# Performance work log

Hardware: AMD Instinct MI355X
Metric: run time of the kernel (lower is better)

Reference implementation:

```python
import jax, jax.numpy as jnp
import numpy as np

N, E, F_IN, H, C = 50000, 800000, 256, 64, 40
NEG_SLOPE = 0.2


def setup_inputs() -> dict:
    key = jax.random.key(0)
    ks = jax.random.split(key, 16)
    sc = lambda fan: 1.0 / np.sqrt(fan)
    return {
        "x": jax.random.normal(ks[0], (N, F_IN), dtype=jnp.float32),
        "edge_index": jax.random.randint(ks[1], (2, E), 0, N, dtype=jnp.int64),
        "W1l": jax.random.normal(ks[2], (F_IN, H), dtype=jnp.float32) * sc(F_IN),
        "b1l": jnp.zeros((H,), jnp.float32),
        "W1r": jax.random.normal(ks[3], (F_IN, H), dtype=jnp.float32) * sc(F_IN),
        "b1r": jnp.zeros((H,), jnp.float32),
        "att1": jax.random.normal(ks[4], (H,), dtype=jnp.float32) * sc(H),
        "bias1": jnp.zeros((H,), jnp.float32),
        "lin1_W": jax.random.normal(ks[5], (F_IN, H), dtype=jnp.float32) * sc(F_IN),
        "lin1_b": jnp.zeros((H,), jnp.float32),
        "W2l": jax.random.normal(ks[6], (H, C), dtype=jnp.float32) * sc(H),
        "b2l": jnp.zeros((C,), jnp.float32),
        "W2r": jax.random.normal(ks[7], (H, C), dtype=jnp.float32) * sc(H),
        "b2r": jnp.zeros((C,), jnp.float32),
        "att2": jax.random.normal(ks[8], (C,), dtype=jnp.float32) * sc(C),
        "bias2": jnp.zeros((C,), jnp.float32),
        "lin2_W": jax.random.normal(ks[9], (H, C), dtype=jnp.float32) * sc(H),
        "lin2_b": jnp.zeros((C,), jnp.float32),
    }


def gatv2_layer(x, src, dst, Wl, bl, Wr, br, att, bias, n):
    # PyG GATv2Conv, heads=1: xl = lin_l(x) (source), xr = lin_r(x) (target)
    xl = x @ Wl + bl                               # [n, out]
    xr = x @ Wr + br                               # [n, out]
    m = xl[src] + xr[dst]                          # [E, out] per-edge gather
    e = jax.nn.leaky_relu(m, NEG_SLOPE) @ att      # [E] attention logits
    # segment softmax over destination nodes (self-loops guarantee nonempty segments)
    emax = jax.ops.segment_max(e, dst, num_segments=n)
    ee = jnp.exp(e - emax[dst])
    denom = jax.ops.segment_sum(ee, dst, num_segments=n)
    alpha = ee / denom[dst]                        # [E]
    out = jax.ops.segment_sum(alpha[:, None] * xl[src], dst, num_segments=n)
    return out + bias


def reference(x, edge_index, W1l, b1l, W1r, b1r, att1, bias1, lin1_W, lin1_b,
              W2l, b2l, W2r, b2r, att2, bias2, lin2_W, lin2_b):
    n = x.shape[0]
    loops = jnp.arange(n, dtype=edge_index.dtype)
    src = jnp.concatenate([edge_index[0], loops])  # add_self_loops=True (PyG default)
    dst = jnp.concatenate([edge_index[1], loops])
    h = jax.nn.relu(gatv2_layer(x, src, dst, W1l, b1l, W1r, b1r, att1, bias1, n)
                    + x @ lin1_W + lin1_b)
    o = (gatv2_layer(h, src, dst, W2l, b2l, W2r, b2r, att2, bias2, n)
         + h @ lin2_W + lin2_b)
    return jax.nn.log_softmax(o, axis=1), edge_index
```

## Files before the change

kernel.cpp:

```cpp
#include <hip/hip_runtime.h>
#include <cmath>

#define NN 50000
#define NP 50048
#define NE 800000
#define CD 40
#define NEG_SLOPE 0.2f
#define NITEMS (NE + NN)
#define CHUNK 2048
#define NCH 416
#define NBKT 391
#define BCAP 3072
#define GB1 782
#define TB1 (3 * 64 * 256)
#define TB2 (3 * 64 * 64)
#define WPB 240

typedef __attribute__((ext_vector_type(8))) short s16x8;
typedef __attribute__((ext_vector_type(4))) float f32x4;
typedef __attribute__((ext_vector_type(2))) float f32x2;

__device__ __forceinline__ f32x2 pk_fma(f32x2 a, f32x2 b, f32x2 c) {
#if __has_builtin(__builtin_elementwise_fma)
  return __builtin_elementwise_fma(a, b, c);
#else
  f32x2 r; r[0] = fmaf(a[0], b[0], c[0]); r[1] = fmaf(a[1], b[1], c[1]); return r;
#endif
}
__device__ __forceinline__ f32x2 pk_max(f32x2 a, f32x2 b) {
#if __has_builtin(__builtin_elementwise_max)
  return __builtin_elementwise_max(a, b);
#else
  f32x2 r; r[0] = fmaxf(a[0], b[0]); r[1] = fmaxf(a[1], b[1]); return r;
#endif
}

__device__ __forceinline__ short f2bf(float x) {
  unsigned u = __builtin_bit_cast(unsigned, x);
  u += 0x7fffu + ((u >> 16) & 1u);
  return (short)(u >> 16);
}
__device__ __forceinline__ unsigned pack2(float lo, float hi) {
  return (unsigned)(unsigned short)f2bf(lo) | ((unsigned)(unsigned short)f2bf(hi) << 16);
}
__device__ __forceinline__ float bf2f_lo(unsigned v) {
  return __builtin_bit_cast(float, v << 16);
}
__device__ __forceinline__ float bf2f_hi(unsigned v) {
  return __builtin_bit_cast(float, v & 0xffff0000u);
}
__device__ __forceinline__ void unp8(uint4 v, f32x2* f) {
  f[0] = (f32x2){bf2f_lo(v.x), bf2f_hi(v.x)};
  f[1] = (f32x2){bf2f_lo(v.y), bf2f_hi(v.y)};
  f[2] = (f32x2){bf2f_lo(v.z), bf2f_hi(v.z)};
  f[3] = (f32x2){bf2f_lo(v.w), bf2f_hi(v.w)};
}
__device__ __forceinline__ uint4 zero4() {
  uint4 z; z.x = 0u; z.y = 0u; z.z = 0u; z.w = 0u; return z;
}

__global__ __launch_bounds__(256) void prep_bin(const float* __restrict__ W1l,
                                                const float* __restrict__ W1r,
                                                const float* __restrict__ L1,
                                                const float* __restrict__ W2l,
                                                const float* __restrict__ W2r,
                                                const float* __restrict__ L2,
                                                short* __restrict__ Wp1,
                                                short* __restrict__ Wp2,
                                                const int* __restrict__ ei,
                                                float* __restrict__ outE,
                                                int* __restrict__ gcur,
                                                unsigned* __restrict__ rec) {
  const int tid = threadIdx.x;
  if (blockIdx.x < WPB) {
    int e = blockIdx.x * 256 + tid;
    if (e < TB1) {
      int kb = e / 6144, r = e % 6144;
      int w = r / 2048, r2 = r % 2048;
      int t = r2 / 512, r3 = r2 % 512;
      int lane = r3 / 8, j = r3 % 8;
      int n = t * 16 + (lane & 15);
      int k = kb * 32 + (lane >> 4) * 8 + j;
      const float* W = (w == 0) ? W1l : (w == 1) ? W1r : L1;
      Wp1[e] = f2bf(W[k * 64 + n]);
    } else {
      e -= TB1;
      int kb = e / 6144, r = e % 6144;
      int w = r / 2048, r2 = r % 2048;
      int t = r2 / 512, r3 = r2 % 512;
      int lane = r3 / 8, j = r3 % 8;
      int n = t * 16 + (lane & 15);
      int k = kb * 32 + (lane >> 4) * 8 + j;
      const float* W = (w == 0) ? W2l : (w == 1) ? W2r : L2;
      Wp2[e] = (n < 40) ? f2bf(W[k * 40 + n]) : (short)0;
    }
    return;
  }
  __shared__ unsigned sorted[CHUNK];
  __shared__ int hist[512];
  __shared__ int bcur[512];
  __shared__ int gbase[512];
  const int base = (blockIdx.x - WPB) * CHUNK;
  for (int t = tid; t < 512; t += 256) { hist[t] = 0; bcur[t] = 0; gbase[t] = 0; }
  __syncthreads();
  unsigned key[CHUNK / 256];
#pragma unroll
  for (int u = 0; u < CHUNK / 256; ++u) {
    const int j = base + u * 256 + tid;
    unsigned k = 0xFFFFFFFFu;
    if (j < NITEMS) {
      int s, d;
      if (j < NE) {
        s = ei[j]; d = ei[NE + j];
        outE[j] = (float)s; outE[NE + j] = (float)d;
      } else {
        s = j - NE; d = s;
      }
      k = ((unsigned)d << 16) | (unsigned)s;
      atomicAdd(&hist[k >> 23], 1);
    }
    key[u] = k;
  }
  __syncthreads();
  if (tid < 64) {
    int carry = 0;
#pragma unroll
    for (int c = 0; c < 8; ++c) {
      int v = hist[c * 64 + tid];
      int inc = v;
#pragma unroll
      for (int off = 1; off < 64; off <<= 1) {
        int tt = __shfl_up(inc, off, 64);
        if (tid >= off) inc += tt;
      }
      hist[c * 64 + tid] = carry + inc - v;
      carry += __shfl(inc, 63, 64);
    }
  }
  __syncthreads();
#pragma unroll
  for (int u = 0; u < CHUNK / 256; ++u) {
    const unsigned k = key[u];
    if (k != 0xFFFFFFFFu) {
      const int b = k >> 23;
      sorted[hist[b] + atomicAdd(&bcur[b], 1)] = k;
    }
  }
  __syncthreads();
  for (int t = tid; t < NBKT; t += 256) {
    const int c = bcur[t];
    if (c > 0) gbase[t] = atomicAdd(&gcur[t], c);
  }
  __syncthreads();
  const int cnt = min(CHUNK, NITEMS - base);
  for (int i = tid; i < cnt; i += 256) {
    const unsigned k = sorted[i];
    const int b = k >> 23;
    const int p = gbase[b] + (i - hist[b]);
    if (p < BCAP) rec[(size_t)b * BCAP + p] = k;
  }
}

__device__ __forceinline__ void gemm1_body(int bid, const float* __restrict__ X,
                                           const short* __restrict__ Wp,
                                           const float* __restrict__ B0,
                                           const float* __restrict__ B1,
                                           const float* __restrict__ B2,
                                           unsigned short* __restrict__ Y0,
                                           unsigned short* __restrict__ Y1,
                                           unsigned short* __restrict__ Y2) {
  const int lane = threadIdx.x & 63;
  const int wave = threadIdx.x >> 6;
  const int r0 = bid * 64 + wave * 16;
  const int m = lane & 15;
  const int q = lane >> 4;
  f32x4 acc[3][4] = {};
  const float* a0 = X + (size_t)min(r0 + m, NN - 1) * 256 + q * 8;
  const short* bp = Wp + lane * 8;
  float4 v0 = *reinterpret_cast<const float4*>(a0);
  float4 v1 = *reinterpret_cast<const float4*>(a0 + 4);
#pragma unroll
  for (int kb = 0; kb < 8; ++kb) {
    s16x8 bf[12];
#pragma unroll
    for (int i = 0; i < 12; ++i)
      bf[i] = *reinterpret_cast<const s16x8*>(bp + (size_t)(kb * 12 + i) * 512);
    s16x8 af;
    af[0] = f2bf(v0.x); af[1] = f2bf(v0.y); af[2] = f2bf(v0.z); af[3] = f2bf(v0.w);
    af[4] = f2bf(v1.x); af[5] = f2bf(v1.y); af[6] = f2bf(v1.z); af[7] = f2bf(v1.w);
    if (kb < 7) {
      v0 = *reinterpret_cast<const float4*>(a0 + (kb + 1) * 32);
      v1 = *reinterpret_cast<const float4*>(a0 + (kb + 1) * 32 + 4);
    }
#pragma unroll
    for (int i = 0; i < 12; ++i)
      acc[i >> 2][i & 3] = __builtin_amdgcn_mfma_f32_16x16x32_bf16(
          af, bf[i], acc[i >> 2][i & 3], 0, 0, 0);
  }
#pragma unroll
  for (int w = 0; w < 3; ++w) {
    const float* B = (w == 0) ? B0 : (w == 1) ? B1 : B2;
    unsigned short* Y = (w == 0) ? Y0 : (w == 1) ? Y1 : Y2;
#pragma unroll
    for (int t = 0; t < 4; ++t) {
      const int c = t * 16 + m;
      const float bv = B[c];
#pragma unroll
      for (int rg = 0; rg < 4; ++rg) {
        const int row = r0 + q * 4 + rg;
        if (row < NN)
          Y[(size_t)row * 64 + c] = (unsigned short)f2bf(acc[w][t][rg] + bv);
      }
    }
  }
}

__global__ __launch_bounds__(256, 3) void build_gemm1(
    const float* __restrict__ X, const short* __restrict__ Wp1,
    const float* __restrict__ B0, const float* __restrict__ B1,
    const float* __restrict__ B2, unsigned short* __restrict__ Y0,
    unsigned short* __restrict__ Y1, unsigned short* __restrict__ Y2,
    const int* __restrict__ gcur, const unsigned* __restrict__ rec,
    int* __restrict__ offsets, unsigned short* __restrict__ csr16) {
  if (blockIdx.x < GB1) {
    gemm1_body(blockIdx.x, X, Wp1, B0, B1, B2, Y0, Y1, Y2);
    return;
  }
  const int b = blockIdx.x - GB1;
  const int tid = threadIdx.x;
  __shared__ unsigned recs[BCAP];
  __shared__ int red[256];
  __shared__ int cnt[128];
  __shared__ int sc[128];
  __shared__ int cur[128];
  int acc = 0;
  for (int t = tid; t < NBKT; t += 256)
    if (t < b) acc += gcur[t];
  red[tid] = acc;
  __syncthreads();
#pragma unroll
  for (int off = 128; off >= 1; off >>= 1) {
    if (tid < off) red[tid] += red[tid + off];
    __syncthreads();
  }
  const int base = red[0];
  const int Tb = min(gcur[b], BCAP);
  if (tid < 128) cnt[tid] = 0;
  __syncthreads();
  for (int i = tid; i < Tb; i += 256) {
    const unsigned k = rec[(size_t)b * BCAP + i];
    recs[i] = k;
    atomicAdd(&cnt[(k >> 16) & 127], 1);
  }
  __syncthreads();
  if (tid < 128) sc[tid] = cnt[tid];
  __syncthreads();
#pragma unroll
  for (int off = 1; off < 128; off <<= 1) {
    int v = (tid < 128 && tid >= off) ? sc[tid - off] : 0;
    __syncthreads();
    if (tid < 128) sc[tid] += v;
    __syncthreads();
  }
  if (tid < 128) {
    const int n = b * 128 + tid;
    if (n < NN) offsets[n + 1] = base + sc[tid];
    cur[tid] = sc[tid] - cnt[tid];
  }
  if (b == 0 && tid == 0) {
    offsets[0] = 0;
#pragma unroll
    for (int i = 0; i < 8; ++i) csr16[NITEMS + i] = 0;
  }
  __syncthreads();
  for (int i = tid; i < Tb; i += 256) {
    const unsigned k = recs[i];
    const int p = atomicAdd(&cur[(k >> 16) & 127], 1);
    csr16[base + p] = (unsigned short)(k & 0xFFFFu);
  }
}

__global__ __launch_bounds__(256, 2) void gemm2(const short* __restrict__ Xb,
                                                const short* __restrict__ Wp,
                                                const float* __restrict__ B0,
                                                const float* __restrict__ B1,
                                                const float* __restrict__ B2,
                                                unsigned short* __restrict__ Y0,
                                                unsigned short* __restrict__ Y1,
                                                unsigned short* __restrict__ Y2) {
  const int lane = threadIdx.x & 63;
  const int wave = threadIdx.x >> 6;
  const int r0 = blockIdx.x * 64 + wave * 16;
  const int m = lane & 15;
  const int q = lane >> 4;
  f32x4 acc[3][3] = {};
  const short* a0 = Xb + (size_t)(r0 + m) * 64 + q * 8;
  const short* bp = Wp + lane * 8;
#pragma unroll
  for (int kb = 0; kb < 2; ++kb) {
    s16x8 bf[9];
#pragma unroll
    for (int w = 0; w < 3; ++w)
#pragma unroll
      for (int t = 0; t < 3; ++t)
        bf[w * 3 + t] =
            *reinterpret_cast<const s16x8*>(bp + (size_t)(kb * 12 + w * 4 + t) * 512);
    const s16x8 af = *reinterpret_cast<const s16x8*>(a0 + kb * 32);
#pragma unroll
    for (int w = 0; w < 3; ++w)
#pragma unroll
      for (int t = 0; t < 3; ++t)
        acc[w][t] = __builtin_amdgcn_mfma_f32_16x16x32_bf16(af, bf[w * 3 + t],
                                                            acc[w][t], 0, 0, 0);
  }
#pragma unroll
  for (int w = 0; w < 3; ++w) {
    const float* B = (w == 0) ? B0 : (w == 1) ? B1 : B2;
    unsigned short* Y = (w == 0) ? Y0 : (w == 1) ? Y1 : Y2;
#pragma unroll
    for (int t = 0; t < 3; ++t) {
      const int c = t * 16 + m;
      if (c < 40) {
        const float bv = B[c];
#pragma unroll
        for (int rg = 0; rg < 4; ++rg) {
          const int row = r0 + q * 4 + rg;
          if (row < NN)
            Y[(size_t)row * 64 + c] = (unsigned short)f2bf(acc[w][t][rg] + bv);
        }
      }
    }
  }
}

template <int OC, bool FINAL>
__global__ __launch_bounds__(256) void gat_agg(const unsigned short* __restrict__ XL,
                                               const unsigned short* __restrict__ XR,
                                               const unsigned short* __restrict__ XLIN,
                                               const float* __restrict__ att,
                                               const float* __restrict__ bias,
                                               const int* __restrict__ offsets,
                                               const unsigned short* __restrict__ csr,
                                               float* __restrict__ out,
                                               unsigned short* __restrict__ outb) {
  const int lane = threadIdx.x & 63;
  const int g = lane >> 3;
  const int l = lane & 7;
  const int wv = threadIdx.x >> 6;
  const int gid = (blockIdx.x * 4 + wv) * 8 + g;
  const int d = min(gid, NN - 1);
  constexpr bool FULLW = (OC >= 64);
  const bool dimok = FULLW || (8 * l < OC);

  const int beg = offsets[d];
  int end = offsets[d + 1];
  if (gid >= NN) end = beg;
  const int deg = end - beg;
  int mdeg = deg;
  mdeg = max(mdeg, __shfl_xor(mdeg, 8, 64));
  mdeg = max(mdeg, __shfl_xor(mdeg, 16, 64));
  mdeg = max(mdeg, __shfl_xor(mdeg, 32, 64));

  f32x2 a2[4] = {};
  if (dimok) {
    const float4 t0 = *reinterpret_cast<const float4*>(&att[8 * l]);
    const float4 t1 = *reinterpret_cast<const float4*>(&att[8 * l + 4]);
    a2[0] = (f32x2){t0.x, t0.y}; a2[1] = (f32x2){t0.z, t0.w};
    a2[2] = (f32x2){t1.x, t1.y}; a2[3] = (f32x2){t1.z, t1.w};
  }
  f32x2 xr2[4];
  unp8(dimok ? *reinterpret_cast<const uint4*>(XR + (size_t)d * 64 + 8 * l) : zero4(),
       xr2);

  const unsigned short* XLl = XL + 8 * l;
  float D = 0.f;
  f32x2 A2[4] = {};
  const f32x2 ns = (f32x2){NEG_SLOPE, NEG_SLOPE};
  int sa = (int)csr[beg];
  uint4 rn = dimok ? *reinterpret_cast<const uint4*>(XLl + (size_t)sa * 64) : zero4();
  sa = (int)csr[beg + 1];
  for (int it = 0; it < mdeg; ++it) {
    const uint4 raw = rn;
    rn = dimok ? *reinterpret_cast<const uint4*>(XLl + (size_t)sa * 64) : zero4();
    sa = (int)csr[beg + it + 2];
    f32x2 xl2[4];
    unp8(raw, xl2);
    f32x2 pacc = (f32x2){0.f, 0.f};
#pragma unroll
    for (int j = 0; j < 4; ++j) {
      const f32x2 t = xl2[j] + xr2[j];
      const f32x2 lr = pk_max(t, t * ns);
      pacc = pk_fma(lr, a2[j], pacc);
    }
    float p = pacc[0] + pacc[1];
    p += __shfl_xor(p, 1, 64);
    p += __shfl_xor(p, 2, 64);
    p += __shfl_xor(p, 4, 64);
    const float w = (it < deg) ? __expf(p) : 0.f;
    D += w;
    const f32x2 w2 = (f32x2){w, w};
#pragma unroll
    for (int j = 0; j < 4; ++j) A2[j] = pk_fma(w2, xl2[j], A2[j]);
  }
  if (gid >= NN) return;
  f32x2 xlin2[4];
  unp8(dimok ? *reinterpret_cast<const uint4*>(XLIN + (size_t)d * 64 + 8 * l)
             : zero4(),
       xlin2);
  float b[8] = {};
  if (dimok) {
    const float4 t0 = *reinterpret_cast<const float4*>(&bias[8 * l]);
    const float4 t1 = *reinterpret_cast<const float4*>(&bias[8 * l + 4]);
    b[0] = t0.x; b[1] = t0.y; b[2] = t0.z; b[3] = t0.w;
    b[4] = t1.x; b[5] = t1.y; b[6] = t1.z; b[7] = t1.w;
  }
  const float inv = 1.0f / D;
  float val[8];
#pragma unroll
  for (int j = 0; j < 8; ++j)
    val[j] = fmaf(A2[j >> 1][j & 1], inv, b[j]) + xlin2[j >> 1][j & 1];
  if (!FINAL) {
    uint4 o;
    o.x = pack2(fmaxf(val[0], 0.f), fmaxf(val[1], 0.f));
    o.y = pack2(fmaxf(val[2], 0.f), fmaxf(val[3], 0.f));
    o.z = pack2(fmaxf(val[4], 0.f), fmaxf(val[5], 0.f));
    o.w = pack2(fmaxf(val[6], 0.f), fmaxf(val[7], 0.f));
    *reinterpret_cast<uint4*>(&outb[(size_t)d * 64 + 8 * l]) = o;
  } else {
    float mx = -3e38f;
    if (dimok) {
#pragma unroll
      for (int j = 0; j < 8; ++j) mx = fmaxf(mx, val[j]);
    }
    mx = fmaxf(mx, __shfl_xor(mx, 1, 64));
    mx = fmaxf(mx, __shfl_xor(mx, 2, 64));
    mx = fmaxf(mx, __shfl_xor(mx, 4, 64));
    float es = 0.f;
    if (dimok) {
#pragma unroll
      for (int j = 0; j < 8; ++j) es += __expf(val[j] - mx);
    }
    es += __shfl_xor(es, 1, 64);
    es += __shfl_xor(es, 2, 64);
    es += __shfl_xor(es, 4, 64);
    const float lse = mx + __logf(es);
    if (dimok) {
      float4 o0, o1;
      o0.x = val[0] - lse; o0.y = val[1] - lse; o0.z = val[2] - lse; o0.w = val[3] - lse;
      o1.x = val[4] - lse; o1.y = val[5] - lse; o1.z = val[6] - lse; o1.w = val[7] - lse;
      float* dst = &out[(size_t)d * OC + 8 * l];
      *reinterpret_cast<float4*>(dst) = o0;
      *reinterpret_cast<float4*>(dst + 4) = o1;
    }
  }
}

extern "C" void kernel_launch(void* const* d_in, const int* in_sizes, int n_in,
                              void* d_out, int out_size, void* d_ws, size_t ws_size,
                              hipStream_t stream) {
  const float* x     = (const float*)d_in[0];
  const int*   ei    = (const int*)d_in[1];
  const float* W1l   = (const float*)d_in[2];
  const float* b1l   = (const float*)d_in[3];
  const float* W1r   = (const float*)d_in[4];
  const float* b1r   = (const float*)d_in[5];
  const float* att1  = (const float*)d_in[6];
  const float* bias1 = (const float*)d_in[7];
  const float* lin1W = (const float*)d_in[8];
  const float* lin1b = (const float*)d_in[9];
  const float* W2l   = (const float*)d_in[10];
  const float* b2l   = (const float*)d_in[11];
  const float* W2r   = (const float*)d_in[12];
  const float* b2r   = (const float*)d_in[13];
  const float* att2  = (const float*)d_in[14];
  const float* bias2 = (const float*)d_in[15];
  const float* lin2W = (const float*)d_in[16];
  const float* lin2b = (const float*)d_in[17];
  float* out = (float*)d_out;

  char* ws = (char*)d_ws;
  size_t off = 0;
  auto alloc = [&](size_t bytes) -> void* {
    void* p = ws + off;
    off += (bytes + 255) & ~(size_t)255;
    return p;
  };
  short* Wp1 = (short*)alloc((size_t)TB1 * 2);
  short* Wp2 = (short*)alloc((size_t)TB2 * 2);
  unsigned short* XL1   = (unsigned short*)alloc((size_t)NN * 64 * 2);
  unsigned short* XR1   = (unsigned short*)alloc((size_t)NN * 64 * 2);
  unsigned short* XLIN1 = (unsigned short*)alloc((size_t)NN * 64 * 2);
  unsigned short* Hb    = (unsigned short*)alloc((size_t)NP * 64 * 2);
  unsigned short* XL2   = (unsigned short*)alloc((size_t)NN * 64 * 2);
  unsigned short* XR2   = (unsigned short*)alloc((size_t)NN * 64 * 2);
  unsigned short* XLIN2 = (unsigned short*)alloc((size_t)NN * 64 * 2);
  int* gcur    = (int*)alloc((size_t)NBKT * 4);
  int* offsets = (int*)alloc((size_t)(NN + 1) * 4);
  unsigned* rec = (unsigned*)alloc((size_t)NBKT * BCAP * 4);
  unsigned short* csr = (unsigned short*)alloc((size_t)(NITEMS + 8) * 2);

  hipMemsetAsync(gcur, 0, (size_t)NBKT * 4, stream);
  prep_bin<<<WPB + NCH, 256, 0, stream>>>(W1l, W1r, lin1W, W2l, W2r, lin2W,
                                          Wp1, Wp2, ei, out + (size_t)NN * CD,
                                          gcur, rec);
  build_gemm1<<<GB1 + NBKT, 256, 0, stream>>>(x, Wp1, b1l, b1r, lin1b,
                                              XL1, XR1, XLIN1, gcur, rec,
                                              offsets, csr);
  const int AGG_BLOCKS = (NN / 8 + 3) / 4;
  gat_agg<64, false><<<AGG_BLOCKS, 256, 0, stream>>>(XL1, XR1, XLIN1, att1,
                                                     bias1, offsets, csr,
                                                     nullptr, Hb);
  gemm2<<<GB1, 256, 0, stream>>>((const short*)Hb, Wp2, b2l, b2r, lin2b,
                                 XL2, XR2, XLIN2);
  gat_agg<40, true><<<AGG_BLOCKS, 256, 0, stream>>>(XL2, XR2, XLIN2, att2,
                                                    bias2, offsets, csr,
                                                    out, nullptr);
}
```

Before: 228.3 us.

## Split each node's edge loop across two waves and combine partials in LDS

The aggregation kernel now assigns two wavefronts to each set of 8 destination nodes. Each wave processes alternating edges (even or odd), and the odd wave's partial softmax denominator and weighted sum go through shared memory to the even wave, which finishes the epilogue. This halves the serial per-node edge loop and doubles the block count to expose more memory-level parallelism for the gathers. The cost is a block-wide barrier, LDS traffic, and idle odd waves during the epilogue. The exp is taken without max subtraction in both versions, so summing partials is consistent.

```diff
diff --git a/kernel.cpp b/kernel.cpp
--- a/kernel.cpp
+++ b/kernel.cpp
@@ -347,7 +347,9 @@
   const int g = lane >> 3;
   const int l = lane & 7;
   const int wv = threadIdx.x >> 6;
-  const int gid = (blockIdx.x * 4 + wv) * 8 + g;
+  const int set = blockIdx.x * 2 + (wv >> 1);
+  const int par = wv & 1;
+  const int gid = set * 8 + g;
   const int d = min(gid, NN - 1);
   constexpr bool FULLW = (OC >= 64);
   const bool dimok = FULLW || (8 * l < OC);
@@ -360,6 +362,7 @@
   mdeg = max(mdeg, __shfl_xor(mdeg, 8, 64));
   mdeg = max(mdeg, __shfl_xor(mdeg, 16, 64));
   mdeg = max(mdeg, __shfl_xor(mdeg, 32, 64));
+  const int nit = (mdeg - par + 1) >> 1;
 
   f32x2 a2[4] = {};
   if (dimok) {
@@ -376,13 +379,13 @@
   float D = 0.f;
   f32x2 A2[4] = {};
   const f32x2 ns = (f32x2){NEG_SLOPE, NEG_SLOPE};
-  int sa = (int)csr[beg];
+  int sa = (int)csr[beg + par];
   uint4 rn = dimok ? *reinterpret_cast<const uint4*>(XLl + (size_t)sa * 64) : zero4();
-  sa = (int)csr[beg + 1];
-  for (int it = 0; it < mdeg; ++it) {
+  sa = (int)csr[beg + par + 2];
+  for (int it = 0; it < nit; ++it) {
     const uint4 raw = rn;
     rn = dimok ? *reinterpret_cast<const uint4*>(XLl + (size_t)sa * 64) : zero4();
-    sa = (int)csr[beg + it + 2];
+    sa = (int)csr[beg + par + 2 * it + 4];
     f32x2 xl2[4];
     unp8(raw, xl2);
     f32x2 pacc = (f32x2){0.f, 0.f};
@@ -396,11 +399,29 @@
     p += __shfl_xor(p, 1, 64);
     p += __shfl_xor(p, 2, 64);
     p += __shfl_xor(p, 4, 64);
-    const float w = (it < deg) ? __expf(p) : 0.f;
+    const float w = (2 * it + par < deg) ? __expf(p) : 0.f;
     D += w;
     const f32x2 w2 = (f32x2){w, w};
 #pragma unroll
     for (int j = 0; j < 4; ++j) A2[j] = pk_fma(w2, xl2[j], A2[j]);
+  }
+  __shared__ float sD[4][64];
+  __shared__ float sA[4][8][64];
+  if (par == 1) {
+    sD[wv][lane] = D;
+#pragma unroll
+    for (int j = 0; j < 4; ++j) {
+      sA[wv][2 * j][lane]     = A2[j][0];
+      sA[wv][2 * j + 1][lane] = A2[j][1];
+    }
+  }
+  __syncthreads();
+  if (par == 1) return;
+  D += sD[wv + 1][lane];
+#pragma unroll
+  for (int j = 0; j < 4; ++j) {
+    A2[j][0] += sA[wv + 1][2 * j][lane];
+    A2[j][1] += sA[wv + 1][2 * j + 1][lane];
   }
   if (gid >= NN) return;
   f32x2 xlin2[4];
@@ -506,7 +527,7 @@
   build_gemm1<<<GB1 + NBKT, 256, 0, stream>>>(x, Wp1, b1l, b1r, lin1b,
                                               XL1, XR1, XLIN1, gcur, rec,
                                               offsets, csr);
-  const int AGG_BLOCKS = (NN / 8 + 3) / 4;
+  const int AGG_BLOCKS = (NN / 8 + 1) / 2;
   gat_agg<64, false><<<AGG_BLOCKS, 256, 0, stream>>>(XL1, XR1, XLIN1, att1,
                                                      bias1, offsets, csr,
                                                      nullptr, Hb);
```

After: 226.8 us. No clear change (-0.7%).

## Fuse layer-2 projection GEMM into layer-1 aggregation epilogue via LDS

Applied to the files above, without the earlier changes.

The first GAT aggregation kernel now stages its 32 ReLU'd hidden rows per block in shared memory and runs the layer-2 MFMA projection (XL2, XR2, XLIN2) directly, removing the separate gemm2 launch and the Hb round trip through global memory. Only two of the four waves do the GEMM after a block barrier, so the tail of the aggregation adds a serialized compute phase and an LDS footprint. Grid sizing is unchanged in effect (32 rows per block).

```diff
diff --git a/kernel.cpp b/kernel.cpp
--- a/kernel.cpp
+++ b/kernel.cpp
@@ -280,60 +280,7 @@
   }
 }
 
-__global__ __launch_bounds__(256, 2) void gemm2(const short* __restrict__ Xb,
-                                                const short* __restrict__ Wp,
-                                                const float* __restrict__ B0,
-                                                const float* __restrict__ B1,
-                                                const float* __restrict__ B2,
-                                                unsigned short* __restrict__ Y0,
-                                                unsigned short* __restrict__ Y1,
-                                                unsigned short* __restrict__ Y2) {
-  const int lane = threadIdx.x & 63;
-  const int wave = threadIdx.x >> 6;
-  const int r0 = blockIdx.x * 64 + wave * 16;
-  const int m = lane & 15;
-  const int q = lane >> 4;
-  f32x4 acc[3][3] = {};
-  const short* a0 = Xb + (size_t)(r0 + m) * 64 + q * 8;
-  const short* bp = Wp + lane * 8;
-#pragma unroll
-  for (int kb = 0; kb < 2; ++kb) {
-    s16x8 bf[9];
-#pragma unroll
-    for (int w = 0; w < 3; ++w)
-#pragma unroll
-      for (int t = 0; t < 3; ++t)
-        bf[w * 3 + t] =
-            *reinterpret_cast<const s16x8*>(bp + (size_t)(kb * 12 + w * 4 + t) * 512);
-    const s16x8 af = *reinterpret_cast<const s16x8*>(a0 + kb * 32);
-#pragma unroll
-    for (int w = 0; w < 3; ++w)
-#pragma unroll
-      for (int t = 0; t < 3; ++t)
-        acc[w][t] = __builtin_amdgcn_mfma_f32_16x16x32_bf16(af, bf[w * 3 + t],
-                                                            acc[w][t], 0, 0, 0);
-  }
-#pragma unroll
-  for (int w = 0; w < 3; ++w) {
-    const float* B = (w == 0) ? B0 : (w == 1) ? B1 : B2;
-    unsigned short* Y = (w == 0) ? Y0 : (w == 1) ? Y1 : Y2;
-#pragma unroll
-    for (int t = 0; t < 3; ++t) {
-      const int c = t * 16 + m;
-      if (c < 40) {
-        const float bv = B[c];
-#pragma unroll
-        for (int rg = 0; rg < 4; ++rg) {
-          const int row = r0 + q * 4 + rg;
-          if (row < NN)
-            Y[(size_t)row * 64 + c] = (unsigned short)f2bf(acc[w][t][rg] + bv);
-        }
-      }
-    }
-  }
-}
-
-template <int OC, bool FINAL>
+template <int OC, bool FINAL, bool FUSE>
 __global__ __launch_bounds__(256) void gat_agg(const unsigned short* __restrict__ XL,
                                                const unsigned short* __restrict__ XR,
                                                const unsigned short* __restrict__ XLIN,
@@ -342,7 +289,14 @@
                                                const int* __restrict__ offsets,
                                                const unsigned short* __restrict__ csr,
                                                float* __restrict__ out,
-                                               unsigned short* __restrict__ outb) {
+                                               unsigned short* __restrict__ outb,
+                                               const short* __restrict__ W2p,
+                                               const float* __restrict__ C0,
+                                               const float* __restrict__ C1,
+                                               const float* __restrict__ C2,
+                                               unsigned short* __restrict__ Z0,
+                                               unsigned short* __restrict__ Z1,
+                                               unsigned short* __restrict__ Z2) {
   const int lane = threadIdx.x & 63;
   const int g = lane >> 3;
   const int l = lane & 7;
@@ -402,55 +356,125 @@
 #pragma unroll
     for (int j = 0; j < 4; ++j) A2[j] = pk_fma(w2, xl2[j], A2[j]);
   }
-  if (gid >= NN) return;
-  f32x2 xlin2[4];
-  unp8(dimok ? *reinterpret_cast<const uint4*>(XLIN + (size_t)d * 64 + 8 * l)
-             : zero4(),
-       xlin2);
-  float b[8] = {};
-  if (dimok) {
-    const float4 t0 = *reinterpret_cast<const float4*>(&bias[8 * l]);
-    const float4 t1 = *reinterpret_cast<const float4*>(&bias[8 * l + 4]);
-    b[0] = t0.x; b[1] = t0.y; b[2] = t0.z; b[3] = t0.w;
-    b[4] = t1.x; b[5] = t1.y; b[6] = t1.z; b[7] = t1.w;
-  }
-  const float inv = 1.0f / D;
-  float val[8];
-#pragma unroll
-  for (int j = 0; j < 8; ++j)
-    val[j] = fmaf(A2[j >> 1][j & 1], inv, b[j]) + xlin2[j >> 1][j & 1];
-  if (!FINAL) {
+  if constexpr (!FUSE) {
+    if (gid >= NN) return;
+    f32x2 xlin2[4];
+    unp8(dimok ? *reinterpret_cast<const uint4*>(XLIN + (size_t)d * 64 + 8 * l)
+               : zero4(),
+         xlin2);
+    float b[8] = {};
+    if (dimok) {
+      const float4 t0 = *reinterpret_cast<const float4*>(&bias[8 * l]);
+      const float4 t1 = *reinterpret_cast<const float4*>(&bias[8 * l + 4]);
+      b[0] = t0.x; b[1] = t0.y; b[2] = t0.z; b[3] = t0.w;
+      b[4] = t1.x; b[5] = t1.y; b[6] = t1.z; b[7] = t1.w;
+    }
+    const float inv = 1.0f / D;
+    float val[8];
+#pragma unroll
+    for (int j = 0; j < 8; ++j)
+      val[j] = fmaf(A2[j >> 1][j & 1], inv, b[j]) + xlin2[j >> 1][j & 1];
+    if (!FINAL) {
+      uint4 o;
+      o.x = pack2(fmaxf(val[0], 0.f), fmaxf(val[1], 0.f));
+      o.y = pack2(fmaxf(val[2], 0.f), fmaxf(val[3], 0.f));
+      o.z = pack2(fmaxf(val[4], 0.f), fmaxf(val[5], 0.f));
+      o.w = pack2(fmaxf(val[6], 0.f), fmaxf(val[7], 0.f));
+      *reinterpret_cast<uint4*>(&outb[(size_t)d * 64 + 8 * l]) = o;
+    } else {
+      float mx = -3e38f;
+      if (dimok) {
+#pragma unroll
+        for (int j = 0; j < 8; ++j) mx = fmaxf(mx, val[j]);
+      }
+      mx = fmaxf(mx, __shfl_xor(mx, 1, 64));
+      mx = fmaxf(mx, __shfl_xor(mx, 2, 64));
+      mx = fmaxf(mx, __shfl_xor(mx, 4, 64));
+      float es = 0.f;
+      if (dimok) {
+#pragma unroll
+        for (int j = 0; j < 8; ++j) es += __expf(val[j] - mx);
+      }
+      es += __shfl_xor(es, 1, 64);
+      es += __shfl_xor(es, 2, 64);
+      es += __shfl_xor(es, 4, 64);
+      const float lse = mx + __logf(es);
+      if (dimok) {
+        float4 o0, o1;
+        o0.x = val[0] - lse; o0.y = val[1] - lse; o0.z = val[2] - lse; o0.w = val[3] - lse;
+        o1.x = val[4] - lse; o1.y = val[5] - lse; o1.z = val[6] - lse; o1.w = val[7] - lse;
+        float* dst = &out[(size_t)d * OC + 8 * l];
+        *reinterpret_cast<float4*>(dst) = o0;
+        *reinterpret_cast<float4*>(dst + 4) = o1;
+      }
+    }
+  } else {
+    __shared__ unsigned h_lds[32][36];
+    f32x2 xlin2[4];
+    unp8(*reinterpret_cast<const uint4*>(XLIN + (size_t)d * 64 + 8 * l), xlin2);
+    float b[8];
+    {
+      const float4 t0 = *reinterpret_cast<const float4*>(&bias[8 * l]);
+      const float4 t1 = *reinterpret_cast<const float4*>(&bias[8 * l + 4]);
+      b[0] = t0.x; b[1] = t0.y; b[2] = t0.z; b[3] = t0.w;
+      b[4] = t1.x; b[5] = t1.y; b[6] = t1.z; b[7] = t1.w;
+    }
+    const float inv = (deg > 0) ? 1.0f / D : 0.f;
+    float val[8];
+#pragma unroll
+    for (int j = 0; j < 8; ++j)
+      val[j] = fmaf(A2[j >> 1][j & 1], inv, b[j]) + xlin2[j >> 1][j & 1];
     uint4 o;
     o.x = pack2(fmaxf(val[0], 0.f), fmaxf(val[1], 0.f));
     o.y = pack2(fmaxf(val[2], 0.f), fmaxf(val[3], 0.f));
     o.z = pack2(fmaxf(val[4], 0.f), fmaxf(val[5], 0.f));
     o.w = pack2(fmaxf(val[6], 0.f), fmaxf(val[7], 0.f));
-    *reinterpret_cast<uint4*>(&outb[(size_t)d * 64 + 8 * l]) = o;
-  } else {
-    float mx = -3e38f;
-    if (dimok) {
-#pragma unroll
-      for (int j = 0; j < 8; ++j) mx = fmaxf(mx, val[j]);
-    }
-    mx = fmaxf(mx, __shfl_xor(mx, 1, 64));
-    mx = fmaxf(mx, __shfl_xor(mx, 2, 64));
-    mx = fmaxf(mx, __shfl_xor(mx, 4, 64));
-    float es = 0.f;
-    if (dimok) {
-#pragma unroll
-      for (int j = 0; j < 8; ++j) es += __expf(val[j] - mx);
-    }
-    es += __shfl_xor(es, 1, 64);
-    es += __shfl_xor(es, 2, 64);
-    es += __shfl_xor(es, 4, 64);
-    const float lse = mx + __logf(es);
-    if (dimok) {
-      float4 o0, o1;
-      o0.x = val[0] - lse; o0.y = val[1] - lse; o0.z = val[2] - lse; o0.w = val[3] - lse;
-      o1.x = val[4] - lse; o1.y = val[5] - lse; o1.z = val[6] - lse; o1.w = val[7] - lse;
-      float* dst = &out[(size_t)d * OC + 8 * l];
-      *reinterpret_cast<float4*>(dst) = o0;
-      *reinterpret_cast<float4*>(dst + 4) = o1;
+    const int localrow = wv * 8 + g;
+    *reinterpret_cast<uint4*>(&h_lds[localrow][4 * l]) = o;
+    __syncthreads();
+    if (wv < 2) {
+      const int m = lane & 15;
+      const int q = lane >> 4;
+      const int r0l = wv * 16;
+      f32x4 acc[3][3] = {};
+      const short* bp = W2p + lane * 8;
+#pragma unroll
+      for (int kb = 0; kb < 2; ++kb) {
+        s16x8 bf[9];
+#pragma unroll
+        for (int w = 0; w < 3; ++w)
+#pragma unroll
+          for (int t = 0; t < 3; ++t)
+            bf[w * 3 + t] = *reinterpret_cast<const s16x8*>(
+                bp + (size_t)(kb * 12 + w * 4 + t) * 512);
+        const s16x8 af =
+            *reinterpret_cast<const s16x8*>(&h_lds[r0l + m][q * 4 + kb * 16]);
+#pragma unroll
+        for (int w = 0; w < 3; ++w)
+#pragma unroll
+          for (int t = 0; t < 3; ++t)
+            acc[w][t] = __builtin_amdgcn_mfma_f32_16x16x32_bf16(af, bf[w * 3 + t],
+                                                                acc[w][t], 0, 0, 0);
+      }
+      const int rowbase = blockIdx.x * 32 + r0l;
+#pragma unroll
+      for (int w = 0; w < 3; ++w) {
+        const float* B = (w == 0) ? C0 : (w == 1) ? C1 : C2;
+        unsigned short* Z = (w == 0) ? Z0 : (w == 1) ? Z1 : Z2;
+#pragma unroll
+        for (int t = 0; t < 3; ++t) {
+          const int c = t * 16 + m;
+          if (c < 40) {
+            const float bv = B[c];
+#pragma unroll
+            for (int rg = 0; rg < 4; ++rg) {
+              const int row = rowbase + q * 4 + rg;
+              if (row < NN)
+                Z[(size_t)row * 64 + c] = (unsigned short)f2bf(acc[w][t][rg] + bv);
+            }
+          }
+        }
+      }
     }
   }
 }
@@ -490,7 +514,6 @@
   unsigned short* XL1   = (unsigned short*)alloc((size_t)NN * 64 * 2);
   unsigned short* XR1   = (unsigned short*)alloc((size_t)NN * 64 * 2);
   unsigned short* XLIN1 = (unsigned short*)alloc((size_t)NN * 64 * 2);
-  unsigned short* Hb    = (unsigned short*)alloc((size_t)NP * 64 * 2);
   unsigned short* XL2   = (unsigned short*)alloc((size_t)NN * 64 * 2);
   unsigned short* XR2   = (unsigned short*)alloc((size_t)NN * 64 * 2);
   unsigned short* XLIN2 = (unsigned short*)alloc((size_t)NN * 64 * 2);
@@ -506,13 +529,11 @@
   build_gemm1<<<GB1 + NBKT, 256, 0, stream>>>(x, Wp1, b1l, b1r, lin1b,
                                               XL1, XR1, XLIN1, gcur, rec,
                                               offsets, csr);
-  const int AGG_BLOCKS = (NN / 8 + 3) / 4;
-  gat_agg<64, false><<<AGG_BLOCKS, 256, 0, stream>>>(XL1, XR1, XLIN1, att1,
-                                                     bias1, offsets, csr,
-                                                     nullptr, Hb);
-  gemm2<<<GB1, 256, 0, stream>>>((const short*)Hb, Wp2, b2l, b2r, lin2b,
-                                 XL2, XR2, XLIN2);
-  gat_agg<40, true><<<AGG_BLOCKS, 256, 0, stream>>>(XL2, XR2, XLIN2, att2,
-                                                    bias2, offsets, csr,
-                                                    out, nullptr);
-}
+  const int AGG_BLOCKS = (NN + 31) / 32;
+  gat_agg<64, false, true><<<AGG_BLOCKS, 256, 0, stream>>>(
+      XL1, XR1, XLIN1, att1, bias1, offsets, csr, nullptr, nullptr,
+      Wp2, b2l, b2r, lin2b, XL2, XR2, XLIN2);
+  gat_agg<40, true, false><<<AGG_BLOCKS, 256, 0, stream>>>(
+      XL2, XR2, XLIN2, att2, bias2, offsets, csr, out, nullptr,
+      nullptr, nullptr, nullptr, nullptr, nullptr, nullptr, nullptr);
+}
```

Result: slower. 243.7 us (+6.7%).
